# Performance work log

Measured on AMD Instinct MI355X. Metric: run time of the kernel, lower is better.

The kernel has to match this reference:

```python
import jax, jax.numpy as jnp
import numpy as np
from jax import lax

KSIZE = 3
SIGMA = 0.8
BLOCK = 8
DCT_THRESH = 2.5
DCT_CLIP = 10.0
DWT_LAM = 0.05


def _gaussian_kernel(dtype):
    coords = jnp.arange(KSIZE, dtype=dtype) - (KSIZE - 1) / 2.0
    grid = coords[None, :] ** 2 + coords[:, None] ** 2
    k = jnp.exp(-grid / (2.0 * SIGMA * SIGMA))
    return k / k.sum()


def gaussian_blur(x):
    # depthwise 3x3 gaussian with reflect padding, groups=C
    C = x.shape[1]
    k = _gaussian_kernel(x.dtype)
    kernel = jnp.broadcast_to(k[None, None], (C, 1, KSIZE, KSIZE))
    pad = KSIZE // 2
    xp = jnp.pad(x, ((0, 0), (0, 0), (pad, pad), (pad, pad)), mode='reflect')
    return lax.conv_general_dilated(
        xp, kernel, window_strides=(1, 1), padding='VALID',
        dimension_numbers=('NCHW', 'OIHW', 'NCHW'), feature_group_count=C)


def block_dct_normalize(x):
    # 8x8 block "DCT" implemented (as in the source) via fft2().real, then
    # soft shrink of small coeffs + clip, then ifft2().real reconstruction.
    B, C, H, W = x.shape
    Ph, Pw = H // BLOCK, W // BLOCK  # H, W chosen as multiples of 8 -> no pad
    blocks = x.reshape(B, C, Ph, BLOCK, Pw, BLOCK).transpose(0, 1, 2, 4, 3, 5)
    coeff = jnp.fft.fft2(blocks, norm='ortho').real
    ca = jnp.abs(coeff)
    coeff = jnp.where(ca < DCT_THRESH, coeff * (ca / (DCT_THRESH + 1e-8)), coeff)
    coeff = jnp.clip(coeff, -DCT_CLIP, DCT_CLIP)
    rec = jnp.fft.ifft2(coeff.astype(jnp.complex64), norm='ortho').real
    rec = rec.transpose(0, 1, 2, 4, 3, 5).reshape(B, C, H, W)
    return rec.astype(x.dtype)


def haar_dwt2(x):
    # orthonormal 2x2 Haar analysis; sign/order conventions cancel in the
    # soft-threshold + inverse pipeline (soft_threshold is odd in sign)
    B, C, H, W = x.shape
    r = x.reshape(B, C, H // 2, 2, W // 2, 2)
    a, b = r[:, :, :, 0, :, 0], r[:, :, :, 0, :, 1]
    c, d = r[:, :, :, 1, :, 0], r[:, :, :, 1, :, 1]
    LL = (a + b + c + d) * 0.5
    LH = (a + b - c - d) * 0.5
    HL = (a - b + c - d) * 0.5
    HH = (a - b - c + d) * 0.5
    return LL, LH, HL, HH


def haar_idwt2(LL, LH, HL, HH):
    B, C, Hh, Wh = LL.shape
    a = (LL + LH + HL + HH) * 0.5
    b = (LL + LH - HL - HH) * 0.5
    c = (LL - LH + HL - HH) * 0.5
    d = (LL - LH - HL + HH) * 0.5
    top = jnp.stack([a, b], axis=-1)  # (B,C,Hh,Wh,2)
    bot = jnp.stack([c, d], axis=-1)
    r = jnp.stack([top, bot], axis=3)  # (B,C,Hh,2,Wh,2)
    return r.reshape(B, C, 2 * Hh, 2 * Wh)


def soft_threshold(x, lam):
    return jnp.sign(x) * jnp.maximum(jnp.abs(x) - lam, 0.0)


def wavelet_refine(x):
    LL, LH, HL, HH = haar_dwt2(x)
    return haar_idwt2(LL, soft_threshold(LH, DWT_LAM),
                      soft_threshold(HL, DWT_LAM),
                      soft_threshold(HH, DWT_LAM))


def setup_inputs() -> dict:
    key = jax.random.key(0)
    I = jax.random.uniform(key, (32, 3, 512, 512), dtype=jnp.float32)
    return {"I": I}


def reference(I):
    I_g = gaussian_blur(I)
    I_d = block_dct_normalize(I_g)
    R_d = I_g - I_d
    I_d_wave = wavelet_refine(I_d)
    R_d_wave = wavelet_refine(R_d)
    # input_mode='concat', residual_type='R_d'
    return jnp.concatenate([I_d_wave, R_d_wave], axis=1)
```

## Files before the change

kernel.cpp:

```cpp
#include <hip/hip_runtime.h>

#define HW 512
#define RA 0.35355339059327373f
#define RB 0.25f

__device__ __forceinline__ int reflect512(int v) {
    v = v < 0 ? -v : v;
    v = v > 511 ? 1022 - v : v;
    return v;
}

__device__ __forceinline__ float softt2(float x) {
    return copysignf(fmaxf(fabsf(x) - 0.1f, 0.0f), x);
}

__device__ __forceinline__ float nlin(float t) {
    float ca = fabsf(t);
    t = (ca < 2.5f) ? t * (ca * 0.4f) : t;
    return fminf(fmaxf(t, -10.0f), 10.0f);
}

__device__ __forceinline__ void haar_quad(float a, float b, float c, float d,
                                          float& oa, float& ob, float& oc, float& od) {
    float s1 = a + b, s2 = c + d, d1 = a - b, d2 = c - d;
    float LL = s1 + s2, LH = s1 - s2, HL = d1 + d2, HH = d1 - d2;
    LH = softt2(LH); HL = softt2(HL); HH = softt2(HH);
    float u1 = LL + LH, u2 = HL + HH, w1 = LL - LH, w2 = HL - HH;
    oa = (u1 + u2) * 0.25f; ob = (u1 - u2) * 0.25f;
    oc = (w1 + w2) * 0.25f; od = (w1 - w2) * 0.25f;
}

__device__ __forceinline__ void cos5(const float* __restrict__ x, float* __restrict__ t) {
    float e0 = x[0] + x[4], d0 = x[0] - x[4];
    float e1 = x[2] + x[6];
    float o0 = x[1] + x[5], m0 = x[1] - x[5];
    float o1 = x[3] + x[7], m1 = x[3] - x[7];
    float see = e0 + e1, dee = e0 - e1, soo = o0 + o1, dd = m0 - m1;
    t[0] = RA * (see + soo);
    t[4] = RA * (see - soo);
    t[2] = RA * dee;
    float a = RA * d0, b = RB * dd;
    t[1] = a + b;
    t[3] = a - b;
}

__device__ __forceinline__ void sin3(const float* __restrict__ x, float* __restrict__ s) {
    float d1 = x[2] - x[6];
    float m0 = x[1] - x[5];
    float o0 = x[1] + x[5];
    float o1 = x[3] + x[7], m1 = x[3] - x[7];
    float qq = m0 + m1;
    float a = RB * qq, b = RA * d1;
    s[0] = a + b;
    s[1] = RA * (o0 - o1);
    s[2] = a - b;
}

__device__ __forceinline__ void cos5_sym(const float* __restrict__ x, float* __restrict__ t) {
    float e0 = x[0] + x[4], d0 = x[0] - x[4];
    float tx2 = 2.0f * x[2];
    float see = e0 + tx2, dee = e0 - tx2;
    float soo = 2.0f * (x[1] + x[3]);
    float m0 = x[1] - x[3];
    t[0] = RA * (see + soo);
    t[4] = RA * (see - soo);
    t[2] = RA * dee;
    float a = RA * d0, b = 0.5f * m0;
    t[1] = a + b;
    t[3] = a - b;
}

__device__ __forceinline__ void sin3_asym(const float* __restrict__ y, float* __restrict__ s) {
    float a = 0.5f * (y[0] + y[2]);
    float b = (2.0f * RA) * y[1];
    s[0] = a + b;
    s[1] = (2.0f * RA) * (y[0] - y[2]);
    s[2] = a - b;
}

__launch_bounds__(256, 3)
__global__ void sas_fused(const float* __restrict__ in, float* __restrict__ out) {
    const int lane = threadIdx.x & 63;
    const int wv = threadIdx.x >> 6;
    const int p = blockIdx.y;
    const int by = blockIdx.x * 4 + wv;
    const float* __restrict__ inP = in + (size_t)p * (HW * HW);
    const int cx = lane * 8;

    const float e = 0.45783336f;
    const float inv_s = 1.0f / ((1.0f + 2.0f * e) * (1.0f + 2.0f * e));

    float4 va[10], vb[10];
#pragma unroll
    for (int j = 0; j < 10; ++j) {
        int gy = reflect512(by * 8 - 1 + j);
        const float* r = inP + (size_t)gy * HW + cx;
        va[j] = *(const float4*)r;
        vb[j] = *(const float4*)(r + 4);
    }

    float h[10][8];
#pragma unroll
    for (int j = 0; j < 10; ++j) {
        float lft = __shfl_up(vb[j].w, 1);
        float rgt = __shfl_down(va[j].x, 1);
        if (lane == 0)  lft = va[j].y;
        if (lane == 63) rgt = vb[j].z;
        float xr[10] = {lft, va[j].x, va[j].y, va[j].z, va[j].w,
                        vb[j].x, vb[j].y, vb[j].z, vb[j].w, rgt};
#pragma unroll
        for (int c = 0; c < 8; ++c)
            h[j][c] = e * (xr[c] + xr[c + 2]) + xr[c + 1];
    }

    float B[8][8];
#pragma unroll
    for (int j = 0; j < 8; ++j)
#pragma unroll
        for (int c = 0; c < 8; ++c)
            B[j][c] = (e * (h[j][c] + h[j + 2][c]) + h[j + 1][c]) * inv_s;

    float cpT[5][8], spT[3][8];
#pragma unroll
    for (int m = 0; m < 8; ++m) {
        float t[5], s[3];
        cos5(B[m], t);
        sin3(B[m], s);
#pragma unroll
        for (int v = 0; v < 5; ++v) cpT[v][m] = t[v];
#pragma unroll
        for (int v = 0; v < 3; ++v) spT[v][m] = s[v];
    }

    float Tc0[5], Tc4[5];
    cos5(cpT[0], Tc0);
    cos5(cpT[4], Tc4);
    float Tt[3], Tb[3], TA[3][3], TB[3][3];
#pragma unroll
    for (int vi = 0; vi < 3; ++vi) {
        float t[5], s[3];
        cos5(cpT[vi + 1], t);
        sin3(spT[vi], s);
        Tt[vi] = t[0];
        Tb[vi] = t[4];
#pragma unroll
        for (int ui = 0; ui < 3; ++ui) {
            TA[vi][ui] = t[ui + 1] - s[ui];
            TB[vi][ui] = t[ui + 1] + s[ui];
        }
    }

#pragma unroll
    for (int i = 0; i < 5; ++i) { Tc0[i] = nlin(Tc0[i]); Tc4[i] = nlin(Tc4[i]); }
#pragma unroll
    for (int vi = 0; vi < 3; ++vi) {
        Tt[vi] = nlin(Tt[vi]);
        Tb[vi] = nlin(Tb[vi]);
#pragma unroll
        for (int ui = 0; ui < 3; ++ui) {
            TA[vi][ui] = nlin(TA[vi][ui]);
            TB[vi][ui] = nlin(TB[vi][ui]);
        }
    }

    float p2[5][5], q2[3][3];
    {
        float x0[5] = {Tc0[0], Tt[0], Tt[1], Tt[2], Tc4[0]};
        cos5_sym(x0, p2[0]);
        float x4[5] = {Tc0[4], Tb[0], Tb[1], Tb[2], Tc4[4]};
        cos5_sym(x4, p2[4]);
    }
#pragma unroll
    for (int u = 1; u <= 3; ++u) {
        float r8[8] = {Tc0[u], TA[0][u - 1], TA[1][u - 1], TA[2][u - 1], Tc4[u],
                       TB[2][u - 1], TB[1][u - 1], TB[0][u - 1]};
        cos5(r8, p2[u]);
        sin3(r8, q2[u - 1]);
    }

    float Rc0[5], Rc4[5];
    {
        float c0[5] = {p2[0][0], p2[1][0], p2[2][0], p2[3][0], p2[4][0]};
        cos5_sym(c0, Rc0);
        float c4[5] = {p2[0][4], p2[1][4], p2[2][4], p2[3][4], p2[4][4]};
        cos5_sym(c4, Rc4);
    }
    float r0v[3], r4v[3], RAm[3][3], RBm[3][3];
#pragma unroll
    for (int vi = 0; vi < 3; ++vi) {
        int v = vi + 1;
        float cs[5] = {p2[0][v], p2[1][v], p2[2][v], p2[3][v], p2[4][v]};
        float t[5];
        cos5_sym(cs, t);
        float y[3] = {q2[0][vi], q2[1][vi], q2[2][vi]};
        float s[3];
        sin3_asym(y, s);
        r0v[vi] = t[0];
        r4v[vi] = t[4];
#pragma unroll
        for (int ui = 0; ui < 3; ++ui) {
            RAm[vi][ui] = t[ui + 1] - s[ui];
            RBm[vi][ui] = t[ui + 1] + s[ui];
        }
    }

    float rec[8][8];
#pragma unroll
    for (int u = 0; u < 8; ++u) {
        int us = (u <= 4) ? u : 8 - u;
        rec[u][0] = Rc0[us];
        rec[u][4] = Rc4[us];
    }
#pragma unroll
    for (int v = 1; v < 8; ++v) {
        if (v == 4) continue;
        int vs = (v <= 4) ? v : 8 - v;
        bool vf = v > 4;
        rec[0][v] = r0v[vs - 1];
        rec[4][v] = r4v[vs - 1];
#pragma unroll
        for (int u = 1; u < 8; ++u) {
            if (u == 4) continue;
            int us = (u <= 4) ? u : 8 - u;
            bool uf = u > 4;
            rec[u][v] = (vf != uf) ? RBm[vs - 1][us - 1] : RAm[vs - 1][us - 1];
        }
    }

    const int chId = (p / 3) * 6 + (p % 3);
    float* __restrict__ oI = out + ((size_t)chId << 18);
    float* __restrict__ oR = out + ((size_t)(chId + 3) << 18);
#pragma unroll
    for (int qy = 0; qy < 4; ++qy) {
        float ti[2][8], tr_[2][8];
#pragma unroll
        for (int qx = 0; qx < 4; ++qx) {
            float d00 = rec[2 * qy][2 * qx],     d01 = rec[2 * qy][2 * qx + 1];
            float d10 = rec[2 * qy + 1][2 * qx], d11 = rec[2 * qy + 1][2 * qx + 1];
            haar_quad(d00, d01, d10, d11,
                      ti[0][2 * qx], ti[0][2 * qx + 1], ti[1][2 * qx], ti[1][2 * qx + 1]);
            float r00 = B[2 * qy][2 * qx]     - d00, r01 = B[2 * qy][2 * qx + 1]     - d01;
            float r10 = B[2 * qy + 1][2 * qx] - d10, r11 = B[2 * qy + 1][2 * qx + 1] - d11;
            haar_quad(r00, r01, r10, r11,
                      tr_[0][2 * qx], tr_[0][2 * qx + 1], tr_[1][2 * qx], tr_[1][2 * qx + 1]);
        }
        size_t base = (size_t)(by * 8 + 2 * qy) * HW + cx;
        *(float4*)&oI[base]          = make_float4(ti[0][0], ti[0][1], ti[0][2], ti[0][3]);
        *(float4*)&oI[base + 4]      = make_float4(ti[0][4], ti[0][5], ti[0][6], ti[0][7]);
        *(float4*)&oI[base + HW]     = make_float4(ti[1][0], ti[1][1], ti[1][2], ti[1][3]);
        *(float4*)&oI[base + HW + 4] = make_float4(ti[1][4], ti[1][5], ti[1][6], ti[1][7]);
        *(float4*)&oR[base]          = make_float4(tr_[0][0], tr_[0][1], tr_[0][2], tr_[0][3]);
        *(float4*)&oR[base + 4]      = make_float4(tr_[0][4], tr_[0][5], tr_[0][6], tr_[0][7]);
        *(float4*)&oR[base + HW]     = make_float4(tr_[1][0], tr_[1][1], tr_[1][2], tr_[1][3]);
        *(float4*)&oR[base + HW + 4] = make_float4(tr_[1][4], tr_[1][5], tr_[1][6], tr_[1][7]);
    }
}

extern "C" void kernel_launch(void* const* d_in, const int* in_sizes, int n_in,
                              void* d_out, int out_size, void* d_ws, size_t ws_size,
                              hipStream_t stream) {
    const float* I = (const float*)d_in[0];
    float* out = (float*)d_out;
    dim3 grid(16, 96);
    sas_fused<<<grid, dim3(256), 0, stream>>>(I, out);
}
```

Before: 281.7 us.

## Reformulate residual via spectral difference to cut live registers and raise occupancy

The blurred block B is no longer kept live for the whole kernel. The residual R = B - rec is rebuilt from the inverse transform of the coefficient differences (t - nlin(t)) plus the stored antisymmetric part of B, which the real-part transform discards. Horizontal blur rows are streamed through a 3-row ring buffer so the forward row transform happens as each row is produced. Launch bounds rise from 3 to 4 waves per SIMD, and a sched_barrier keeps all loads ahead of compute. In exchange the inverse transform now runs twice, which adds ALU work, and forcing 4 waves may cause register spills.

```diff
diff --git a/kernel.cpp b/kernel.cpp
--- a/kernel.cpp
+++ b/kernel.cpp
@@ -78,114 +78,31 @@
     s[2] = a - b;
 }
 
-__launch_bounds__(256, 3)
-__global__ void sas_fused(const float* __restrict__ in, float* __restrict__ out) {
-    const int lane = threadIdx.x & 63;
-    const int wv = threadIdx.x >> 6;
-    const int p = blockIdx.y;
-    const int by = blockIdx.x * 4 + wv;
-    const float* __restrict__ inP = in + (size_t)p * (HW * HW);
-    const int cx = lane * 8;
-
-    const float e = 0.45783336f;
-    const float inv_s = 1.0f / ((1.0f + 2.0f * e) * (1.0f + 2.0f * e));
-
-    float4 va[10], vb[10];
-#pragma unroll
-    for (int j = 0; j < 10; ++j) {
-        int gy = reflect512(by * 8 - 1 + j);
-        const float* r = inP + (size_t)gy * HW + cx;
-        va[j] = *(const float4*)r;
-        vb[j] = *(const float4*)(r + 4);
-    }
-
-    float h[10][8];
-#pragma unroll
-    for (int j = 0; j < 10; ++j) {
-        float lft = __shfl_up(vb[j].w, 1);
-        float rgt = __shfl_down(va[j].x, 1);
-        if (lane == 0)  lft = va[j].y;
-        if (lane == 63) rgt = vb[j].z;
-        float xr[10] = {lft, va[j].x, va[j].y, va[j].z, va[j].w,
-                        vb[j].x, vb[j].y, vb[j].z, vb[j].w, rgt};
-#pragma unroll
-        for (int c = 0; c < 8; ++c)
-            h[j][c] = e * (xr[c] + xr[c + 2]) + xr[c + 1];
-    }
-
-    float B[8][8];
-#pragma unroll
-    for (int j = 0; j < 8; ++j)
-#pragma unroll
-        for (int c = 0; c < 8; ++c)
-            B[j][c] = (e * (h[j][c] + h[j + 2][c]) + h[j + 1][c]) * inv_s;
-
-    float cpT[5][8], spT[3][8];
-#pragma unroll
-    for (int m = 0; m < 8; ++m) {
-        float t[5], s[3];
-        cos5(B[m], t);
-        sin3(B[m], s);
-#pragma unroll
-        for (int v = 0; v < 5; ++v) cpT[v][m] = t[v];
-#pragma unroll
-        for (int v = 0; v < 3; ++v) spT[v][m] = s[v];
-    }
-
-    float Tc0[5], Tc4[5];
-    cos5(cpT[0], Tc0);
-    cos5(cpT[4], Tc4);
-    float Tt[3], Tb[3], TA[3][3], TB[3][3];
-#pragma unroll
-    for (int vi = 0; vi < 3; ++vi) {
-        float t[5], s[3];
-        cos5(cpT[vi + 1], t);
-        sin3(spT[vi], s);
-        Tt[vi] = t[0];
-        Tb[vi] = t[4];
-#pragma unroll
-        for (int ui = 0; ui < 3; ++ui) {
-            TA[vi][ui] = t[ui + 1] - s[ui];
-            TB[vi][ui] = t[ui + 1] + s[ui];
-        }
-    }
-
-#pragma unroll
-    for (int i = 0; i < 5; ++i) { Tc0[i] = nlin(Tc0[i]); Tc4[i] = nlin(Tc4[i]); }
-#pragma unroll
-    for (int vi = 0; vi < 3; ++vi) {
-        Tt[vi] = nlin(Tt[vi]);
-        Tb[vi] = nlin(Tb[vi]);
-#pragma unroll
-        for (int ui = 0; ui < 3; ++ui) {
-            TA[vi][ui] = nlin(TA[vi][ui]);
-            TB[vi][ui] = nlin(TB[vi][ui]);
-        }
-    }
-
+__device__ __forceinline__ void inverse34(
+    const float c0[5], const float c4[5], const float tt[3], const float bb[3],
+    const float A[3][3], const float Bm[3][3],
+    float Rc0[5], float Rc4[5], float r0v[3], float r4v[3],
+    float RAm[3][3], float RBm[3][3]) {
     float p2[5][5], q2[3][3];
     {
-        float x0[5] = {Tc0[0], Tt[0], Tt[1], Tt[2], Tc4[0]};
+        float x0[5] = {c0[0], tt[0], tt[1], tt[2], c4[0]};
         cos5_sym(x0, p2[0]);
-        float x4[5] = {Tc0[4], Tb[0], Tb[1], Tb[2], Tc4[4]};
+        float x4[5] = {c0[4], bb[0], bb[1], bb[2], c4[4]};
         cos5_sym(x4, p2[4]);
     }
 #pragma unroll
     for (int u = 1; u <= 3; ++u) {
-        float r8[8] = {Tc0[u], TA[0][u - 1], TA[1][u - 1], TA[2][u - 1], Tc4[u],
-                       TB[2][u - 1], TB[1][u - 1], TB[0][u - 1]};
+        float r8[8] = {c0[u], A[0][u - 1], A[1][u - 1], A[2][u - 1], c4[u],
+                       Bm[2][u - 1], Bm[1][u - 1], Bm[0][u - 1]};
         cos5(r8, p2[u]);
         sin3(r8, q2[u - 1]);
     }
-
-    float Rc0[5], Rc4[5];
-    {
-        float c0[5] = {p2[0][0], p2[1][0], p2[2][0], p2[3][0], p2[4][0]};
-        cos5_sym(c0, Rc0);
-        float c4[5] = {p2[0][4], p2[1][4], p2[2][4], p2[3][4], p2[4][4]};
-        cos5_sym(c4, Rc4);
-    }
-    float r0v[3], r4v[3], RAm[3][3], RBm[3][3];
+    {
+        float cc0[5] = {p2[0][0], p2[1][0], p2[2][0], p2[3][0], p2[4][0]};
+        cos5_sym(cc0, Rc0);
+        float cc4[5] = {p2[0][4], p2[1][4], p2[2][4], p2[3][4], p2[4][4]};
+        cos5_sym(cc4, Rc4);
+    }
 #pragma unroll
     for (int vi = 0; vi < 3; ++vi) {
         int v = vi + 1;
@@ -203,8 +120,11 @@
             RBm[vi][ui] = t[ui + 1] + s[ui];
         }
     }
-
-    float rec[8][8];
+}
+
+__device__ __forceinline__ void expand34(
+    const float Rc0[5], const float Rc4[5], const float r0v[3], const float r4v[3],
+    const float RAm[3][3], const float RBm[3][3], float rec[8][8]) {
 #pragma unroll
     for (int u = 0; u < 8; ++u) {
         int us = (u <= 4) ? u : 8 - u;
@@ -226,33 +146,162 @@
             rec[u][v] = (vf != uf) ? RBm[vs - 1][us - 1] : RAm[vs - 1][us - 1];
         }
     }
+}
+
+__device__ __forceinline__ void haar_store(const float rec[8][8],
+                                           float* __restrict__ o, int by, int cx) {
+#pragma unroll
+    for (int qy = 0; qy < 4; ++qy) {
+        float ti[2][8];
+#pragma unroll
+        for (int qx = 0; qx < 4; ++qx) {
+            haar_quad(rec[2 * qy][2 * qx], rec[2 * qy][2 * qx + 1],
+                      rec[2 * qy + 1][2 * qx], rec[2 * qy + 1][2 * qx + 1],
+                      ti[0][2 * qx], ti[0][2 * qx + 1], ti[1][2 * qx], ti[1][2 * qx + 1]);
+        }
+        size_t base = (size_t)(by * 8 + 2 * qy) * HW + cx;
+        *(float4*)&o[base]          = make_float4(ti[0][0], ti[0][1], ti[0][2], ti[0][3]);
+        *(float4*)&o[base + 4]      = make_float4(ti[0][4], ti[0][5], ti[0][6], ti[0][7]);
+        *(float4*)&o[base + HW]     = make_float4(ti[1][0], ti[1][1], ti[1][2], ti[1][3]);
+        *(float4*)&o[base + HW + 4] = make_float4(ti[1][4], ti[1][5], ti[1][6], ti[1][7]);
+    }
+}
+
+__launch_bounds__(256, 4)
+__global__ void sas_fused(const float* __restrict__ in, float* __restrict__ out) {
+    const int lane = threadIdx.x & 63;
+    const int wv = threadIdx.x >> 6;
+    const int p = blockIdx.y;
+    const int by = blockIdx.x * 4 + wv;
+    const float* __restrict__ inP = in + (size_t)p * (HW * HW);
+    const int cx = lane * 8;
+
+    const float e = 0.45783336f;
+    const float inv_s = 1.0f / ((1.0f + 2.0f * e) * (1.0f + 2.0f * e));
+
+    float4 va[10], vb[10];
+#pragma unroll
+    for (int j = 0; j < 10; ++j) {
+        int gy = reflect512(by * 8 - 1 + j);
+        const float* r = inP + (size_t)gy * HW + cx;
+        va[j] = *(const float4*)r;
+        vb[j] = *(const float4*)(r + 4);
+    }
+    __builtin_amdgcn_sched_barrier(0);
+
+    float cpT[5][8], spT[3][8];
+    float Ba0[3], Ba4[3];
+    float Ba[3][8];
+    float Bs[3][8];
+    {
+        float h[3][8];
+#pragma unroll
+        for (int j = 0; j < 10; ++j) {
+            float lft = __shfl_up(vb[j].w, 1);
+            float rgt = __shfl_down(va[j].x, 1);
+            if (lane == 0)  lft = va[j].y;
+            if (lane == 63) rgt = vb[j].z;
+            float xr[10] = {lft, va[j].x, va[j].y, va[j].z, va[j].w,
+                            vb[j].x, vb[j].y, vb[j].z, vb[j].w, rgt};
+            float* hc = h[j % 3];
+#pragma unroll
+            for (int c = 0; c < 8; ++c)
+                hc[c] = e * (xr[c] + xr[c + 2]) + xr[c + 1];
+            if (j >= 2) {
+                const float* h0 = h[(j - 2) % 3];
+                const float* h1 = h[(j - 1) % 3];
+                float Brow[8];
+#pragma unroll
+                for (int c = 0; c < 8; ++c)
+                    Brow[c] = (e * (h0[c] + hc[c]) + h1[c]) * inv_s;
+                const int m = j - 2;
+                float t[5], s[3];
+                cos5(Brow, t);
+                sin3(Brow, s);
+#pragma unroll
+                for (int v = 0; v < 5; ++v) cpT[v][m] = t[v];
+#pragma unroll
+                for (int v = 0; v < 3; ++v) spT[v][m] = s[v];
+                if (m == 0) {
+#pragma unroll
+                    for (int v = 1; v <= 3; ++v) Ba0[v - 1] = (Brow[v] - Brow[8 - v]) * 0.5f;
+                } else if (m == 4) {
+#pragma unroll
+                    for (int v = 1; v <= 3; ++v) Ba4[v - 1] = (Brow[v] - Brow[8 - v]) * 0.5f;
+                } else if (m <= 3) {
+#pragma unroll
+                    for (int c = 0; c < 8; ++c) Bs[m - 1][c] = Brow[c];
+                } else {
+                    const int u = 8 - m;
+#pragma unroll
+                    for (int v = 0; v < 8; ++v)
+                        Ba[u - 1][v] = (Bs[u - 1][v] - Brow[(8 - v) & 7]) * 0.5f;
+                }
+            }
+        }
+    }
+
+    float Tc0[5], Tc4[5], Dc0[5], Dc4[5];
+    {
+        float t[5];
+        cos5(cpT[0], t);
+#pragma unroll
+        for (int i = 0; i < 5; ++i) { float tn = nlin(t[i]); Tc0[i] = tn; Dc0[i] = t[i] - tn; }
+        cos5(cpT[4], t);
+#pragma unroll
+        for (int i = 0; i < 5; ++i) { float tn = nlin(t[i]); Tc4[i] = tn; Dc4[i] = t[i] - tn; }
+    }
+    float Tt[3], Tb[3], TA[3][3], TBm[3][3];
+    float Dt[3], Db[3], DA[3][3], DBm[3][3];
+#pragma unroll
+    for (int vi = 0; vi < 3; ++vi) {
+        float t[5], s[3];
+        cos5(cpT[vi + 1], t);
+        sin3(spT[vi], s);
+        { float x = t[0]; float tn = nlin(x); Tt[vi] = tn; Dt[vi] = x - tn; }
+        { float x = t[4]; float tn = nlin(x); Tb[vi] = tn; Db[vi] = x - tn; }
+#pragma unroll
+        for (int ui = 0; ui < 3; ++ui) {
+            float xa = t[ui + 1] - s[ui];
+            float na = nlin(xa);
+            TA[vi][ui] = na; DA[vi][ui] = xa - na;
+            float xb = t[ui + 1] + s[ui];
+            float nb = nlin(xb);
+            TBm[vi][ui] = nb; DBm[vi][ui] = xb - nb;
+        }
+    }
 
     const int chId = (p / 3) * 6 + (p % 3);
     float* __restrict__ oI = out + ((size_t)chId << 18);
     float* __restrict__ oR = out + ((size_t)(chId + 3) << 18);
-#pragma unroll
-    for (int qy = 0; qy < 4; ++qy) {
-        float ti[2][8], tr_[2][8];
-#pragma unroll
-        for (int qx = 0; qx < 4; ++qx) {
-            float d00 = rec[2 * qy][2 * qx],     d01 = rec[2 * qy][2 * qx + 1];
-            float d10 = rec[2 * qy + 1][2 * qx], d11 = rec[2 * qy + 1][2 * qx + 1];
-            haar_quad(d00, d01, d10, d11,
-                      ti[0][2 * qx], ti[0][2 * qx + 1], ti[1][2 * qx], ti[1][2 * qx + 1]);
-            float r00 = B[2 * qy][2 * qx]     - d00, r01 = B[2 * qy][2 * qx + 1]     - d01;
-            float r10 = B[2 * qy + 1][2 * qx] - d10, r11 = B[2 * qy + 1][2 * qx + 1] - d11;
-            haar_quad(r00, r01, r10, r11,
-                      tr_[0][2 * qx], tr_[0][2 * qx + 1], tr_[1][2 * qx], tr_[1][2 * qx + 1]);
-        }
-        size_t base = (size_t)(by * 8 + 2 * qy) * HW + cx;
-        *(float4*)&oI[base]          = make_float4(ti[0][0], ti[0][1], ti[0][2], ti[0][3]);
-        *(float4*)&oI[base + 4]      = make_float4(ti[0][4], ti[0][5], ti[0][6], ti[0][7]);
-        *(float4*)&oI[base + HW]     = make_float4(ti[1][0], ti[1][1], ti[1][2], ti[1][3]);
-        *(float4*)&oI[base + HW + 4] = make_float4(ti[1][4], ti[1][5], ti[1][6], ti[1][7]);
-        *(float4*)&oR[base]          = make_float4(tr_[0][0], tr_[0][1], tr_[0][2], tr_[0][3]);
-        *(float4*)&oR[base + 4]      = make_float4(tr_[0][4], tr_[0][5], tr_[0][6], tr_[0][7]);
-        *(float4*)&oR[base + HW]     = make_float4(tr_[1][0], tr_[1][1], tr_[1][2], tr_[1][3]);
-        *(float4*)&oR[base + HW + 4] = make_float4(tr_[1][4], tr_[1][5], tr_[1][6], tr_[1][7]);
+
+    {
+        float Rc0[5], Rc4[5], r0v[3], r4v[3], RAm[3][3], RBm[3][3];
+        inverse34(Dc0, Dc4, Dt, Db, DA, DBm, Rc0, Rc4, r0v, r4v, RAm, RBm);
+        float rec[8][8];
+        expand34(Rc0, Rc4, r0v, r4v, RAm, RBm, rec);
+#pragma unroll
+        for (int v = 1; v <= 3; ++v) {
+            rec[0][v] += Ba0[v - 1];
+            rec[0][8 - v] -= Ba0[v - 1];
+            rec[4][v] += Ba4[v - 1];
+            rec[4][8 - v] -= Ba4[v - 1];
+        }
+#pragma unroll
+        for (int u = 1; u <= 3; ++u)
+#pragma unroll
+            for (int v = 0; v < 8; ++v) {
+                rec[u][v] += Ba[u - 1][v];
+                rec[8 - u][(8 - v) & 7] -= Ba[u - 1][v];
+            }
+        haar_store(rec, oR, by, cx);
+    }
+    {
+        float Rc0[5], Rc4[5], r0v[3], r4v[3], RAm[3][3], RBm[3][3];
+        inverse34(Tc0, Tc4, Tt, Tb, TA, TBm, Rc0, Rc4, r0v, r4v, RAm, RBm);
+        float rec[8][8];
+        expand34(Rc0, Rc4, r0v, r4v, RAm, RBm, rec);
+        haar_store(rec, oI, by, cx);
     }
 }
 
```

Result: slower. 336.9 us (+19.6%).
